# Performance work log

Measured on AMD Instinct MI355X. Metric: run time of the kernel, lower is better.

Reference implementation:

```python
import jax, jax.numpy as jnp
import numpy as np

EMBED_DIM = 1024
NUM_HEADS = 16
HEAD_DIM = EMBED_DIM // NUM_HEADS


def setup_inputs() -> dict:
    key = jax.random.key(0)
    ks = jax.random.split(key, 5)
    B, S, E = 2, 2048, EMBED_DIM
    # xavier-uniform-ish scale for square linear weights
    lim = float(np.sqrt(6.0 / (E + E)))
    x = jax.random.normal(ks[0], (B, S, E), dtype=jnp.float32)
    Wq = jax.random.uniform(ks[1], (E, E), jnp.float32, -lim, lim)
    Wk = jax.random.uniform(ks[2], (E, E), jnp.float32, -lim, lim)
    Wv = jax.random.uniform(ks[3], (E, E), jnp.float32, -lim, lim)
    Wo = jax.random.uniform(ks[4], (E, E), jnp.float32, -lim, lim)
    z = jnp.zeros((E,), jnp.float32)
    return {"x": x, "Wq": Wq, "bq": z, "Wk": Wk, "bk": z,
            "Wv": Wv, "bv": z, "Wo": Wo, "bo": z}


def reference(x, Wq, bq, Wk, bk, Wv, bv, Wo, bo):
    B, S, E = x.shape
    H, Dh = NUM_HEADS, HEAD_DIM
    # Linear projections (torch Linear: y = x @ W.T + b)
    q = (x @ Wq.T + bq).reshape(B, S, H, Dh).transpose(0, 2, 1, 3)  # [B,H,S,Dh]
    k = (x @ Wk.T + bk).reshape(B, S, H, Dh).transpose(0, 2, 1, 3)
    v = (x @ Wv.T + bv).reshape(B, S, H, Dh).transpose(0, 2, 1, 3)
    # NOTE: module scales by 1/head_dim (not 1/sqrt(head_dim)) — faithful.
    logits = jnp.einsum('bhqd,bhkd->bhqk', q, k) / Dh  # [B,H,S,S]
    attn = jax.nn.softmax(logits, axis=-1)
    vals = jnp.einsum('bhqk,bhkd->bhqd', attn, v)      # [B,H,S,Dh]
    vals = vals.transpose(0, 2, 1, 3).reshape(B, S, E)
    out = vals @ Wo.T + bo
    return out
```

## Files before the change

kernel.cpp:

```cpp
#include <hip/hip_runtime.h>
#include <hip/hip_bf16.h>

#define EDIM 1024
#define NH   16
#define DH   64
#define BB   2
#define SS   2048
#define MM   (BB*SS)

typedef unsigned short u16;
typedef unsigned int   u32;
typedef __attribute__((ext_vector_type(4)))  float f32x4;
typedef __attribute__((ext_vector_type(16))) float f32x16;
typedef __attribute__((ext_vector_type(8)))  short s16x8;

__device__ __forceinline__ u16 f2bf(float x) {
    __hip_bfloat16 b = __float2bfloat16(x);
    return *(u16*)&b;
}
__device__ __forceinline__ u32 cvtpk(float lo, float hi_) {
    u32 r;
    asm("v_cvt_pk_bf16_f32 %0, %1, %2" : "=v"(r) : "v"(lo), "v"(hi_));
    return r;
}
__device__ __forceinline__ void swap32(u32& a, u32& b) {
    asm("v_permlane32_swap_b32 %0, %1" : "+v"(a), "+v"(b));
}

__device__ __forceinline__ void gload16(const void* g, void* l) {
    __builtin_amdgcn_global_load_lds(
        (const __attribute__((address_space(1))) unsigned int*)g,
        (__attribute__((address_space(3))) unsigned int*)l, 16, 0, 0);
}

#define QSCALE 0.0225421209f

__global__ __launch_bounds__(256) void convert_all(const float* __restrict__ x,
                                                   const float* __restrict__ Wq,
                                                   const float* __restrict__ Wk,
                                                   const float* __restrict__ Wv,
                                                   const float* __restrict__ Wo,
                                                   u16* __restrict__ xh,
                                                   u16* __restrict__ wqkv,
                                                   u16* __restrict__ woh)
{
    const int i = blockIdx.x * 256 + threadIdx.x;
    const float* src; ushort4* dst; int off;
    if (i < 1048576)      { src = x;  dst = (ushort4*)xh;   off = i; }
    else if (i < 1310720) { src = Wq; dst = (ushort4*)wqkv; off = i - 1048576; }
    else if (i < 1572864) { src = Wk; dst = (ushort4*)wqkv; off = i - 1310720 + 262144; }
    else if (i < 1835008) { src = Wv; dst = (ushort4*)wqkv; off = i - 1572864 + 524288; }
    else                  { src = Wo; dst = (ushort4*)woh;  off = i - 1835008; }
    const int so = (i < 1048576) ? i
                 : (i < 1310720) ? (i - 1048576)
                 : (i < 1572864) ? (i - 1310720)
                 : (i < 1835008) ? (i - 1572864) : (i - 1835008);
    const float4 v = ((const float4*)src)[so];
    ushort4 h;
    h.x = f2bf(v.x); h.y = f2bf(v.y); h.z = f2bf(v.z); h.w = f2bf(v.w);
    dst[off] = h;
}

__global__ __launch_bounds__(256) void gemm_qkv(const u16* __restrict__ A,
                                                const u16* __restrict__ B,
                                                const float* __restrict__ bq,
                                                const float* __restrict__ bk,
                                                const float* __restrict__ bv,
                                                u16* __restrict__ qb,
                                                u16* __restrict__ kb,
                                                u16* __restrict__ vT)
{
    __shared__ __align__(16) u16 As[128][64];
    __shared__ __align__(16) u16 Bs[128][64];

    const int tid  = threadIdx.x;
    const int lane = tid & 63, wid = tid >> 6;
    const int wm = wid >> 1, wn = wid & 1;
    const int swz = (blockIdx.x & 7) * 96 + (blockIdx.x >> 3);
    const int m0 = (swz & 31) * 128;
    const int n0 = (swz >> 5) * 128;

    size_t aoff[4], boff[4];
    #pragma unroll
    for (int i = 0; i < 4; ++i) {
        const int flat = i * 256 + tid;
        const int row = flat >> 3, u = flat & 7;
        const size_t o = (size_t)row * 2048 + ((u ^ (row & 7)) << 4);
        aoff[i] = o; boff[i] = o;
    }
    const char* Abase = (const char*)(A + (size_t)m0 * 1024);
    const char* Bbase = (const char*)(B + (size_t)n0 * 1024);

    f32x4 acc[4][4];
    #pragma unroll
    for (int i = 0; i < 4; ++i)
        #pragma unroll
        for (int j = 0; j < 4; ++j) acc[i][j] = f32x4{0.f, 0.f, 0.f, 0.f};

    #pragma unroll 1
    for (int t = 0; t < 16; ++t) {
        const size_t kb_ = (size_t)t * 128;
        #pragma unroll
        for (int i = 0; i < 4; ++i)
            gload16(Abase + aoff[i] + kb_, (char*)As + (i * 256 + wid * 64) * 16);
        #pragma unroll
        for (int i = 0; i < 4; ++i)
            gload16(Bbase + boff[i] + kb_, (char*)Bs + (i * 256 + wid * 64) * 16);
        __syncthreads();

        #pragma unroll
        for (int kk = 0; kk < 2; ++kk) {
            s16x8 af[4], bfr[4];
            #pragma unroll
            for (int i = 0; i < 4; ++i) {
                const int rowA = wm * 64 + i * 16 + (lane & 15);
                af[i] = *(const s16x8*)((const char*)As + rowA * 128 + (((kk * 4 + (lane >> 4)) ^ (rowA & 7)) << 4));
                const int rowB = wn * 64 + i * 16 + (lane & 15);
                bfr[i] = *(const s16x8*)((const char*)Bs + rowB * 128 + (((kk * 4 + (lane >> 4)) ^ (rowB & 7)) << 4));
            }
            #pragma unroll
            for (int i = 0; i < 4; ++i)
                #pragma unroll
                for (int j = 0; j < 4; ++j)
                    acc[i][j] = __builtin_amdgcn_mfma_f32_16x16x32_bf16(af[i], bfr[j], acc[i][j], 0, 0, 0);
        }
        __syncthreads();
    }

    if (n0 < 1024) {
        #pragma unroll
        for (int i = 0; i < 4; ++i) {
            const int mbase = m0 + wm * 64 + i * 16 + ((lane >> 4) * 4);
            #pragma unroll
            for (int j = 0; j < 4; ++j) {
                const int n = n0 + wn * 64 + j * 16 + (lane & 15);
                const float bias = bq[n];
                const int h_ = n >> 6, d_ = n & 63;
                #pragma unroll
                for (int r = 0; r < 4; ++r) {
                    const int m = mbase + r;
                    const int b_ = m >> 11, s_ = m & 2047;
                    qb[((size_t)(b_ * NH + h_) * SS + s_) * DH + d_] =
                        f2bf((acc[i][j][r] + bias) * QSCALE);
                }
            }
        }
    } else if (n0 < 2048) {
        #pragma unroll
        for (int i = 0; i < 4; ++i) {
            const int mbase = m0 + wm * 64 + i * 16 + ((lane >> 4) * 4);
            #pragma unroll
            for (int j = 0; j < 4; ++j) {
                const int n = n0 + wn * 64 + j * 16 + (lane & 15);
                const float bias = bk[n - 1024];
                const int h_ = (n >> 6) & 15, d_ = n & 63;
                #pragma unroll
                for (int r = 0; r < 4; ++r) {
                    const int m = mbase + r;
                    const int b_ = m >> 11, s_ = m & 2047;
                    kb[((size_t)(b_ * NH + h_) * SS + s_) * DH + d_] = f2bf(acc[i][j][r] + bias);
                }
            }
        }
    } else {
        #pragma unroll
        for (int i = 0; i < 4; ++i) {
            const int mbase = m0 + wm * 64 + i * 16 + ((lane >> 4) * 4);
            #pragma unroll
            for (int j = 0; j < 4; ++j) {
                const int n = n0 + wn * 64 + j * 16 + (lane & 15);
                const float bias = bv[n - 2048];
                const int hd = n - 2048;
                #pragma unroll
                for (int r = 0; r < 4; ++r) {
                    const int m = mbase + r;
                    const int b_ = m >> 11, s_ = m & 2047;
                    vT[((size_t)(b_ * EDIM) + hd) * SS + s_] = f2bf(acc[i][j][r] + bias);
                }
            }
        }
    }
}

__global__ __launch_bounds__(256) void gemm_out(const u16* __restrict__ A,
                                                const u16* __restrict__ B,
                                                const float* __restrict__ bo,
                                                float* __restrict__ out)
{
    __shared__ __align__(16) u16 As[64][64];
    __shared__ __align__(16) u16 Bs[128][64];

    const int tid  = threadIdx.x;
    const int lane = tid & 63, wid = tid >> 6;
    const int wm = wid >> 1, wn = wid & 1;
    const int swz = (blockIdx.x & 7) * 64 + (blockIdx.x >> 3);
    const int m0 = (swz & 63) * 64;
    const int n0 = (swz >> 6) * 128;

    size_t aoff[2], boff[4];
    #pragma unroll
    for (int i = 0; i < 2; ++i) {
        const int flat = i * 256 + tid;
        const int row = flat >> 3, u = flat & 7;
        aoff[i] = (size_t)row * 2048 + ((u ^ (row & 7)) << 4);
    }
    #pragma unroll
    for (int i = 0; i < 4; ++i) {
        const int flat = i * 256 + tid;
        const int row = flat >> 3, u = flat & 7;
        boff[i] = (size_t)row * 2048 + ((u ^ (row & 7)) << 4);
    }
    const char* Abase = (const char*)(A + (size_t)m0 * 1024);
    const char* Bbase = (const char*)(B + (size_t)n0 * 1024);

    f32x4 acc[2][4];
    #pragma unroll
    for (int i = 0; i < 2; ++i)
        #pragma unroll
        for (int j = 0; j < 4; ++j) acc[i][j] = f32x4{0.f, 0.f, 0.f, 0.f};

    #pragma unroll 1
    for (int t = 0; t < 16; ++t) {
        const size_t kb_ = (size_t)t * 128;
        #pragma unroll
        for (int i = 0; i < 2; ++i)
            gload16(Abase + aoff[i] + kb_, (char*)As + (i * 256 + wid * 64) * 16);
        #pragma unroll
        for (int i = 0; i < 4; ++i)
            gload16(Bbase + boff[i] + kb_, (char*)Bs + (i * 256 + wid * 64) * 16);
        __syncthreads();

        #pragma unroll
        for (int kk = 0; kk < 2; ++kk) {
            s16x8 af[2], bfr[4];
            #pragma unroll
            for (int i = 0; i < 2; ++i) {
                const int rowA = wm * 32 + i * 16 + (lane & 15);
                af[i] = *(const s16x8*)((const char*)As + rowA * 128 + (((kk * 4 + (lane >> 4)) ^ (rowA & 7)) << 4));
            }
            #pragma unroll
            for (int j = 0; j < 4; ++j) {
                const int rowB = wn * 64 + j * 16 + (lane & 15);
                bfr[j] = *(const s16x8*)((const char*)Bs + rowB * 128 + (((kk * 4 + (lane >> 4)) ^ (rowB & 7)) << 4));
            }
            #pragma unroll
            for (int i = 0; i < 2; ++i)
                #pragma unroll
                for (int j = 0; j < 4; ++j)
                    acc[i][j] = __builtin_amdgcn_mfma_f32_16x16x32_bf16(af[i], bfr[j], acc[i][j], 0, 0, 0);
        }
        __syncthreads();
    }

    #pragma unroll
    for (int i = 0; i < 2; ++i) {
        const int mbase = m0 + wm * 32 + i * 16 + ((lane >> 4) * 4);
        #pragma unroll
        for (int j = 0; j < 4; ++j) {
            const int n = n0 + wn * 64 + j * 16 + (lane & 15);
            #pragma unroll
            for (int r = 0; r < 4; ++r)
                out[(size_t)(mbase + r) * EDIM + n] = acc[i][j][r] + bo[n];
        }
    }
}

__global__ __launch_bounds__(256) void attn_mfma(const u16* __restrict__ q,
                                                 const u16* __restrict__ k,
                                                 const u16* __restrict__ vT,
                                                 u16* __restrict__ valsh)
{
    __shared__ __align__(16) u16 kt[128][64];
    __shared__ __align__(16) u16 vt[64][128];

    const int tid = threadIdx.x, lane = tid & 63, wid = tid >> 6;
    const int lq = lane & 31, hi = lane >> 5;
    const int swz = (blockIdx.x & 7) * 64 + (blockIdx.x >> 3);
    const int bh = swz >> 4, qt = swz & 15;
    const int b = bh >> 4, h = bh & 15;

    const u16* qg = q + ((size_t)bh * SS + qt * 128 + wid * 32 + lq) * DH + hi * 8;
    s16x8 qf[4];
    #pragma unroll
    for (int ks = 0; ks < 4; ++ks) qf[ks] = *(const s16x8*)(qg + ks * 16);

    f32x16 acc_o[2];
    #pragma unroll
    for (int db = 0; db < 2; ++db)
        #pragma unroll
        for (int r = 0; r < 16; ++r) acc_o[db][r] = 0.f;
    float rs = 0.f;

    const char* kbh = (const char*)(k + (size_t)bh * SS * DH);
    const char* vbh = (const char*)(vT + ((size_t)b * EDIM + h * DH) * SS);
    const char* ksrc[4]; const char* vsrc[4];
    #pragma unroll
    for (int i = 0; i < 4; ++i) {
        const int flat = i * 256 + tid;
        const int row = flat >> 3, u = flat & 7;
        const int su = u ^ (row & 7) ^ ((row >> 3) & 3);
        ksrc[i] = kbh + (size_t)row * 128 + (su << 4);
        const int rowv = flat >> 4, uv = flat & 15;
        const int suv = uv ^ (rowv & 15) ^ ((rowv & 16) >> 2);
        vsrc[i] = vbh + (size_t)rowv * (SS * 2) + (suv << 4);
    }

    #pragma unroll 1
    for (int c = 0; c < 16; ++c) {
        #pragma unroll
        for (int i = 0; i < 4; ++i) {
            gload16(ksrc[i], (char*)kt + (i * 256 + wid * 64) * 16);
            ksrc[i] += 128 * 128;
        }
        #pragma unroll
        for (int i = 0; i < 4; ++i) {
            gload16(vsrc[i], (char*)vt + (i * 256 + wid * 64) * 16);
            vsrc[i] += 256;
        }
        __syncthreads();

        #pragma unroll
        for (int kb = 0; kb < 4; ++kb) {
            f32x16 sc;
            #pragma unroll
            for (int r = 0; r < 16; ++r) sc[r] = 0.f;
            const int krow = kb * 32 + lq;
            __builtin_amdgcn_s_setprio(1);
            #pragma unroll
            for (int ks = 0; ks < 4; ++ks) {
                const int u = (ks * 2 + hi) ^ (krow & 7) ^ ((krow >> 3) & 3);
                const s16x8 kf = *(const s16x8*)((const char*)kt + krow * 128 + u * 16);
                sc = __builtin_amdgcn_mfma_f32_32x32x16_bf16(kf, qf[ks], sc, 0, 0, 0);
            }
            __builtin_amdgcn_s_setprio(0);

            #pragma unroll
            for (int r = 0; r < 16; ++r) {
                sc[r] = __builtin_amdgcn_exp2f(sc[r]);
                rs += sc[r];
            }

            u32 w0 = cvtpk(sc[0],  sc[1]),  w1 = cvtpk(sc[2],  sc[3]);
            u32 w2 = cvtpk(sc[4],  sc[5]),  w3 = cvtpk(sc[6],  sc[7]);
            u32 w4 = cvtpk(sc[8],  sc[9]),  w5 = cvtpk(sc[10], sc[11]);
            u32 w6 = cvtpk(sc[12], sc[13]), w7 = cvtpk(sc[14], sc[15]);
            swap32(w0, w2);
            swap32(w1, w3);
            swap32(w4, w6);
            swap32(w5, w7);
            union { u32 w[4]; s16x8 v; } pa0, pa1;
            pa0.w[0] = w0; pa0.w[1] = w1; pa0.w[2] = w2; pa0.w[3] = w3;
            pa1.w[0] = w4; pa1.w[1] = w5; pa1.w[2] = w6; pa1.w[3] = w7;

            __builtin_amdgcn_s_setprio(1);
            #pragma unroll
            for (int t = 0; t < 2; ++t) {
                const s16x8 pat = t ? pa1.v : pa0.v;
                const int kst = kb * 2 + t;
                #pragma unroll
                for (int db = 0; db < 2; ++db) {
                    const int vrow = db * 32 + lq;
                    const int u = (kst * 2 + hi) ^ (vrow & 15) ^ ((vrow & 16) >> 2);
                    const s16x8 vf = *(const s16x8*)((const char*)vt + vrow * 256 + u * 16);
                    acc_o[db] = __builtin_amdgcn_mfma_f32_32x32x16_bf16(pat, vf, acc_o[db], 0, 0, 0);
                }
            }
            __builtin_amdgcn_s_setprio(0);
        }
        __syncthreads();
    }

    const float rsf = rs + __shfl_xor(rs, 32, 64);
    const float inv = 1.f / rsf;
    float iv[16];
    #pragma unroll
    for (int r = 0; r < 16; ++r)
        iv[r] = __shfl(inv, (r & 3) + 8 * (r >> 2) + 4 * hi, 64);

    #pragma unroll
    for (int db = 0; db < 2; ++db)
        #pragma unroll
        for (int r = 0; r < 16; ++r) {
            const int srow = qt * 128 + wid * 32 + (r & 3) + 8 * (r >> 2) + 4 * hi;
            const int col  = h * 64 + db * 32 + lq;
            valsh[(size_t)(b * SS + srow) * EDIM + col] = f2bf(acc_o[db][r] * iv[r]);
        }
}

extern "C" void kernel_launch(void* const* d_in, const int* in_sizes, int n_in,
                              void* d_out, int out_size, void* d_ws, size_t ws_size,
                              hipStream_t stream)
{
    const float* x  = (const float*)d_in[0];
    const float* Wq = (const float*)d_in[1];
    const float* bq = (const float*)d_in[2];
    const float* Wk = (const float*)d_in[3];
    const float* bk = (const float*)d_in[4];
    const float* Wv = (const float*)d_in[5];
    const float* bv = (const float*)d_in[6];
    const float* Wo = (const float*)d_in[7];
    const float* bo = (const float*)d_in[8];
    float* out = (float*)d_out;

    u16* W = (u16*)d_ws;
    const size_t M1 = 1024 * 1024;
    u16* xh    = W;
    u16* wqkv  = W + 4  * M1;
    u16* woh   = W + 7  * M1;
    u16* qbuf  = W + 8  * M1;
    u16* kbuf  = W + 12 * M1;
    u16* vbufT = W + 16 * M1;
    u16* valsh = W + 20 * M1;

    convert_all<<<dim3(8192), 256, 0, stream>>>(x, Wq, Wk, Wv, Wo, xh, wqkv, woh);

    gemm_qkv<<<dim3(768), 256, 0, stream>>>(xh, wqkv, bq, bk, bv, qbuf, kbuf, vbufT);

    attn_mfma<<<dim3(BB * NH * (SS / 128)), 256, 0, stream>>>(qbuf, kbuf, vbufT, valsh);

    gemm_out<<<dim3(512), 256, 0, stream>>>(valsh, woh, bo, out);
}
```

Baseline: 200.0 us.

## Double-buffer K/V tiles and process two query blocks per wave in attention

```diff
diff --git a/kernel.cpp b/kernel.cpp
--- a/kernel.cpp
+++ b/kernel.cpp
@@ -270,26 +270,31 @@
                                                  const u16* __restrict__ vT,
                                                  u16* __restrict__ valsh)
 {
-    __shared__ __align__(16) u16 kt[128][64];
-    __shared__ __align__(16) u16 vt[64][128];
+    __shared__ __align__(16) u16 kt[2][128][64];
+    __shared__ __align__(16) u16 vt[2][64][128];
 
     const int tid = threadIdx.x, lane = tid & 63, wid = tid >> 6;
     const int lq = lane & 31, hi = lane >> 5;
-    const int swz = (blockIdx.x & 7) * 64 + (blockIdx.x >> 3);
-    const int bh = swz >> 4, qt = swz & 15;
+    const int swz = (blockIdx.x & 7) * 32 + (blockIdx.x >> 3);
+    const int bh = swz >> 3, qt = swz & 7;
     const int b = bh >> 4, h = bh & 15;
 
-    const u16* qg = q + ((size_t)bh * SS + qt * 128 + wid * 32 + lq) * DH + hi * 8;
-    s16x8 qf[4];
-    #pragma unroll
-    for (int ks = 0; ks < 4; ++ks) qf[ks] = *(const s16x8*)(qg + ks * 16);
-
-    f32x16 acc_o[2];
-    #pragma unroll
-    for (int db = 0; db < 2; ++db)
-        #pragma unroll
-        for (int r = 0; r < 16; ++r) acc_o[db][r] = 0.f;
-    float rs = 0.f;
+    s16x8 qf[2][4];
+    #pragma unroll
+    for (int mi = 0; mi < 2; ++mi) {
+        const u16* qg = q + ((size_t)bh * SS + qt * 256 + wid * 64 + mi * 32 + lq) * DH + hi * 8;
+        #pragma unroll
+        for (int ks = 0; ks < 4; ++ks) qf[mi][ks] = *(const s16x8*)(qg + ks * 16);
+    }
+
+    f32x16 acc_o[2][2];
+    #pragma unroll
+    for (int mi = 0; mi < 2; ++mi)
+        #pragma unroll
+        for (int db = 0; db < 2; ++db)
+            #pragma unroll
+            for (int r = 0; r < 16; ++r) acc_o[mi][db][r] = 0.f;
+    float rs[2] = {0.f, 0.f};
 
     const char* kbh = (const char*)(k + (size_t)bh * SS * DH);
     const char* vbh = (const char*)(vT + ((size_t)b * EDIM + h * DH) * SS);
@@ -305,86 +310,107 @@
         vsrc[i] = vbh + (size_t)rowv * (SS * 2) + (suv << 4);
     }
 
+    auto stage = [&](int buf) {
+        #pragma unroll
+        for (int i = 0; i < 4; ++i) {
+            gload16(ksrc[i], (char*)kt + buf * 16384 + (i * 256 + wid * 64) * 16);
+            ksrc[i] += 128 * 128;
+        }
+        #pragma unroll
+        for (int i = 0; i < 4; ++i) {
+            gload16(vsrc[i], (char*)vt + buf * 16384 + (i * 256 + wid * 64) * 16);
+            vsrc[i] += 256;
+        }
+    };
+
+    stage(0);
+    __syncthreads();
+
+    int buf = 0;
     #pragma unroll 1
     for (int c = 0; c < 16; ++c) {
-        #pragma unroll
-        for (int i = 0; i < 4; ++i) {
-            gload16(ksrc[i], (char*)kt + (i * 256 + wid * 64) * 16);
-            ksrc[i] += 128 * 128;
-        }
-        #pragma unroll
-        for (int i = 0; i < 4; ++i) {
-            gload16(vsrc[i], (char*)vt + (i * 256 + wid * 64) * 16);
-            vsrc[i] += 256;
-        }
-        __syncthreads();
+        if (c < 15) stage(buf ^ 1);
+        const char* ktb = (const char*)kt + buf * 16384;
+        const char* vtb = (const char*)vt + buf * 16384;
 
         #pragma unroll
         for (int kb = 0; kb < 4; ++kb) {
-            f32x16 sc;
-            #pragma unroll
-            for (int r = 0; r < 16; ++r) sc[r] = 0.f;
+            f32x16 sc0, sc1;
+            #pragma unroll
+            for (int r = 0; r < 16; ++r) { sc0[r] = 0.f; sc1[r] = 0.f; }
             const int krow = kb * 32 + lq;
             __builtin_amdgcn_s_setprio(1);
             #pragma unroll
             for (int ks = 0; ks < 4; ++ks) {
                 const int u = (ks * 2 + hi) ^ (krow & 7) ^ ((krow >> 3) & 3);
-                const s16x8 kf = *(const s16x8*)((const char*)kt + krow * 128 + u * 16);
-                sc = __builtin_amdgcn_mfma_f32_32x32x16_bf16(kf, qf[ks], sc, 0, 0, 0);
+                const s16x8 kf = *(const s16x8*)(ktb + krow * 128 + u * 16);
+                sc0 = __builtin_amdgcn_mfma_f32_32x32x16_bf16(kf, qf[0][ks], sc0, 0, 0, 0);
+                sc1 = __builtin_amdgcn_mfma_f32_32x32x16_bf16(kf, qf[1][ks], sc1, 0, 0, 0);
             }
             __builtin_amdgcn_s_setprio(0);
 
             #pragma unroll
             for (int r = 0; r < 16; ++r) {
-                sc[r] = __builtin_amdgcn_exp2f(sc[r]);
-                rs += sc[r];
-            }
-
-            u32 w0 = cvtpk(sc[0],  sc[1]),  w1 = cvtpk(sc[2],  sc[3]);
-            u32 w2 = cvtpk(sc[4],  sc[5]),  w3 = cvtpk(sc[6],  sc[7]);
-            u32 w4 = cvtpk(sc[8],  sc[9]),  w5 = cvtpk(sc[10], sc[11]);
-            u32 w6 = cvtpk(sc[12], sc[13]), w7 = cvtpk(sc[14], sc[15]);
-            swap32(w0, w2);
-            swap32(w1, w3);
-            swap32(w4, w6);
-            swap32(w5, w7);
-            union { u32 w[4]; s16x8 v; } pa0, pa1;
-            pa0.w[0] = w0; pa0.w[1] = w1; pa0.w[2] = w2; pa0.w[3] = w3;
-            pa1.w[0] = w4; pa1.w[1] = w5; pa1.w[2] = w6; pa1.w[3] = w7;
+                sc0[r] = __builtin_amdgcn_exp2f(sc0[r]);
+                rs[0] += sc0[r];
+                sc1[r] = __builtin_amdgcn_exp2f(sc1[r]);
+                rs[1] += sc1[r];
+            }
+
+            s16x8 pav[2][2];
+            #pragma unroll
+            for (int mi = 0; mi < 2; ++mi) {
+                const f32x16& sc = mi ? sc1 : sc0;
+                u32 w0 = cvtpk(sc[0],  sc[1]),  w1 = cvtpk(sc[2],  sc[3]);
+                u32 w2 = cvtpk(sc[4],  sc[5]),  w3 = cvtpk(sc[6],  sc[7]);
+                u32 w4 = cvtpk(sc[8],  sc[9]),  w5 = cvtpk(sc[10], sc[11]);
+                u32 w6 = cvtpk(sc[12], sc[13]), w7 = cvtpk(sc[14], sc[15]);
+                swap32(w0, w2);
+                swap32(w1, w3);
+                swap32(w4, w6);
+                swap32(w5, w7);
+                union { u32 w[4]; s16x8 v; } p0, p1;
+                p0.w[0] = w0; p0.w[1] = w1; p0.w[2] = w2; p0.w[3] = w3;
+                p1.w[0] = w4; p1.w[1] = w5; p1.w[2] = w6; p1.w[3] = w7;
+                pav[mi][0] = p0.v; pav[mi][1] = p1.v;
+            }
 
             __builtin_amdgcn_s_setprio(1);
             #pragma unroll
             for (int t = 0; t < 2; ++t) {
-                const s16x8 pat = t ? pa1.v : pa0.v;
                 const int kst = kb * 2 + t;
                 #pragma unroll
                 for (int db = 0; db < 2; ++db) {
                     const int vrow = db * 32 + lq;
                     const int u = (kst * 2 + hi) ^ (vrow & 15) ^ ((vrow & 16) >> 2);
-                    const s16x8 vf = *(const s16x8*)((const char*)vt + vrow * 256 + u * 16);
-                    acc_o[db] = __builtin_amdgcn_mfma_f32_32x32x16_bf16(pat, vf, acc_o[db], 0, 0, 0);
+                    const s16x8 vf = *(const s16x8*)(vtb + vrow * 256 + u * 16);
+                    acc_o[0][db] = __builtin_amdgcn_mfma_f32_32x32x16_bf16(pav[0][t], vf, acc_o[0][db], 0, 0, 0);
+                    acc_o[1][db] = __builtin_amdgcn_mfma_f32_32x32x16_bf16(pav[1][t], vf, acc_o[1][db], 0, 0, 0);
                 }
             }
             __builtin_amdgcn_s_setprio(0);
         }
         __syncthreads();
-    }
-
-    const float rsf = rs + __shfl_xor(rs, 32, 64);
-    const float inv = 1.f / rsf;
-    float iv[16];
-    #pragma unroll
-    for (int r = 0; r < 16; ++r)
-        iv[r] = __shfl(inv, (r & 3) + 8 * (r >> 2) + 4 * hi, 64);
-
-    #pragma unroll
-    for (int db = 0; db < 2; ++db)
-        #pragma unroll
-        for (int r = 0; r < 16; ++r) {
-            const int srow = qt * 128 + wid * 32 + (r & 3) + 8 * (r >> 2) + 4 * hi;
-            const int col  = h * 64 + db * 32 + lq;
-            valsh[(size_t)(b * SS + srow) * EDIM + col] = f2bf(acc_o[db][r] * iv[r]);
-        }
+        buf ^= 1;
+    }
+
+    #pragma unroll
+    for (int mi = 0; mi < 2; ++mi) {
+        const float rsf = rs[mi] + __shfl_xor(rs[mi], 32, 64);
+        const float inv = 1.f / rsf;
+        float iv[16];
+        #pragma unroll
+        for (int r = 0; r < 16; ++r)
+            iv[r] = __shfl(inv, (r & 3) + 8 * (r >> 2) + 4 * hi, 64);
+        #pragma unroll
+        for (int db = 0; db < 2; ++db)
+            #pragma unroll
+            for (int r = 0; r < 16; ++r) {
+                const int srow = qt * 256 + wid * 64 + mi * 32 + (r & 3) + 8 * (r >> 2) + 4 * hi;
+                const int col  = h * 64 + db * 32 + lq;
+                valsh[(size_t)(b * SS + srow) * EDIM + col] = f2bf(acc_o[mi][db][r] * iv[r]);
+            }
+    }
 }
 
 extern "C" void kernel_launch(void* const* d_in, const int* in_sizes, int n_in,
@@ -416,7 +442,7 @@
 
     gemm_qkv<<<dim3(768), 256, 0, stream>>>(xh, wqkv, bq, bk, bv, qbuf, kbuf, vbufT);
 
-    attn_mfma<<<dim3(BB * NH * (SS / 128)), 256, 0, stream>>>(qbuf, kbuf, vbufT, valsh);
+    attn_mfma<<<dim3(256), 256, 0, stream>>>(qbuf, kbuf, vbufT, valsh);
 
     gemm_out<<<dim3(512), 256, 0, stream>>>(valsh, woh, bo, out);
 }
```

After: 211.4 us. 1.06x slower.
